# Optimization experiments

Measured on AMD Instinct MI355X. Metric: run time of the kernel, lower is better.

Reference implementation:

```python
import jax, jax.numpy as jnp
import numpy as np

H, W = 3000, 3000

def setup_inputs() -> dict:
    rng = np.random.default_rng(0)
    activities_np = rng.random((H, W)) < 0.9
    nb_active = int(activities_np.sum())
    vertex_weights = jnp.asarray(rng.random((H, W), dtype=np.float32))
    neighbors = jnp.array([(1, 0), (-1, 0), (0, 1), (0, -1)], dtype=jnp.int32)  # rook contiguity
    return {
        "activities": jnp.asarray(activities_np),
        "vertex_weights": vertex_weights,
        "neighbors": neighbors,
        "nb_active": nb_active,
    }


def reference(activities, vertex_weights, neighbors, nb_active):
    nrows, ncols = activities.shape
    num_nodes = nb_active  # static python int
    # active vertex index -> (i, j) coords, row-major order (matches jnp.nonzero)
    rows, cols = jnp.nonzero(activities, size=num_nodes)
    source_xy = jnp.stack([rows, cols], axis=1)  # [N, 2]
    # (i, j) -> active vertex index map, -1 for inactive
    active_map = jnp.full((nrows, ncols), -1, dtype=jnp.int32)
    active_map = active_map.at[rows, cols].set(jnp.arange(num_nodes, dtype=jnp.int32))
    # candidate neighbor coordinates [N, K, 2]
    cand = source_xy[:, None, :] + neighbors[None, :, :].astype(source_xy.dtype)
    ci_raw, cj_raw = cand[..., 0], cand[..., 1]
    in_bounds = (ci_raw >= 0) & (ci_raw < nrows) & (cj_raw >= 0) & (cj_raw < ncols)
    ci = jnp.clip(ci_raw, 0, nrows - 1)
    cj = jnp.clip(cj_raw, 0, ncols - 1)
    target_active = activities[ci, cj]
    valid = in_bounds & target_active  # [N, K]
    # zero out invalid coords before gather (matches original)
    vi = jnp.where(valid, ci_raw, 0)
    vj = jnp.where(valid, cj_raw, 0)
    tgt = jnp.where(valid, active_map[vi, vj], 0)
    src = jnp.where(valid, jnp.arange(num_nodes, dtype=jnp.int32)[:, None], 0)
    vals = jnp.where(valid, vertex_weights[vi, vj], 0.0)
    indices = jnp.stack([src.ravel(), tgt.ravel()], axis=1)  # [N*K, 2]
    return vals.ravel(), indices  # BCOO data and indices, shape (num_nodes, num_nodes)
```

## Files before the change

### kernel.cpp

```cpp
#include <hip/hip_runtime.h>
#include <cstdint>

#define HH 3000
#define WW 3000
#define WPR 48
#define NW (HH * WPR)

typedef unsigned long long u64;
typedef float f4v __attribute__((ext_vector_type(4)));

#define BITS_OFF 0
#define ROWS_OFF 1152000
#define P_OFF    1164032

__device__ __forceinline__ void nt_store4(float a, float b, float c, float d, float4* p) {
    f4v x; x.x = a; x.y = b; x.z = c; x.w = d;
    __builtin_nontemporal_store(x, (f4v*)p);
}

__device__ __forceinline__ int detect_mode(const void* acts, int t, int lane, int wv,
                                           int* s_red, int* s_mode) {
    int v = (int)((const unsigned*)acts)[t];
    #pragma unroll
    for (int off = 32; off > 0; off >>= 1) v = max(v, __shfl_down(v, off));
    if (lane == 0) s_red[wv] = v;
    __syncthreads();
    if (t == 0) {
        int mx = max(max(s_red[0], s_red[1]), max(s_red[2], s_red[3]));
        *s_mode = (mx > 1 && mx <= 0x01010101) ? 1 : 0;
    }
    __syncthreads();
    return *s_mode;
}

__global__ __launch_bounds__(256) void k_build(const void* __restrict__ acts,
                                               u64* __restrict__ bits,
                                               int* __restrict__ rowSums) {
    __shared__ int s_red[4];
    __shared__ int s_mode;
    const int t = threadIdx.x, lane = t & 63, wv = t >> 6;
    const int mode = detect_mode(acts, t, lane, wv, s_red, &s_mode);

    const int r = blockIdx.x;
    const long rowbase = (long)r * WW;
    int mycnt = 0;
    for (int it = 0; it < 12; ++it) {
        int wi = it * 4 + wv;
        int j = wi * 64 + lane;
        bool a = false;
        if (j < WW) {
            if (mode) a = ((const unsigned char*)acts)[rowbase + j] != 0;
            else      a = ((const unsigned*)acts)[rowbase + j] != 0u;
        }
        u64 m = __ballot(a);
        if (lane == 0) {
            bits[r * WPR + wi] = m;
            mycnt += __popcll(m);
        }
    }
    if (lane == 0) s_red[wv] = mycnt;
    __syncthreads();
    if (t == 0) rowSums[r] = s_red[0] + s_red[1] + s_red[2] + s_red[3];
}

__global__ __launch_bounds__(256) void k_prefixP(const u64* __restrict__ bits,
                                                 const int* __restrict__ rowSums,
                                                 int* __restrict__ P) {
    __shared__ int s_red[4];
    const int t = threadIdx.x, lane = t & 63, wv = t >> 6;
    const int r0 = blockIdx.x * 4;
    int s = 0;
    for (int idx = t; idx < r0; idx += 256) s += rowSums[idx];
    #pragma unroll
    for (int off = 32; off > 0; off >>= 1) s += __shfl_down(s, off);
    if (lane == 0) s_red[wv] = s;
    __syncthreads();
    int base = s_red[0] + s_red[1] + s_red[2] + s_red[3];

    const int r = r0 + wv;
    if (r < HH) {
        int rbase = base;
        if (wv >= 1) rbase += rowSums[r0];
        if (wv >= 2) rbase += rowSums[r0 + 1];
        if (wv >= 3) rbase += rowSums[r0 + 2];
        const int w = r * WPR + lane;
        int v = (lane < WPR) ? __popcll(bits[w]) : 0;
        int x = v;
        #pragma unroll
        for (int off = 1; off < 64; off <<= 1) {
            int y = __shfl_up(x, off);
            if (lane >= off) x += y;
        }
        if (lane < WPR) P[w] = rbase + (x - v);
    }
}

__global__ __launch_bounds__(256) void k_emit(const u64* __restrict__ bits,
                                              const int* __restrict__ P,
                                              const float* __restrict__ wts,
                                              float* __restrict__ out, int N) {
    const int t = threadIdx.x;
    const int lane = t & 63;
    const int wv = t >> 6;
    const int i = blockIdx.y;

    float4* valsg = (float4*)out;
    float4* indsg = (float4*)(out + (size_t)N * 4);

    #pragma unroll
    for (int half = 0; half < 2; ++half) {
        const int wi = blockIdx.x * 8 + half * 4 + wv;
        const int j = wi * 64 + lane;
        const int w = i * WPR + wi;
        const u64 mself = bits[w];
        if (!((mself >> lane) & 1ull)) continue;

        const int v = P[w] + __popcll(mself & ((1ull << lane) - 1ull));
        const float nf = (float)v;
        const long c = (long)i * WW + j;

        float val0, val1, val2, val3, sf0, sf1, sf2, sf3, tf0, tf1, tf2, tf3;
        {
            bool ok = (i < HH - 1);
            u64 wd = ok ? bits[w + WPR] : 0ull;
            bool aa = ok && ((wd >> lane) & 1ull);
            val0 = aa ? wts[c + WW] : 0.f; sf0 = aa ? nf : 0.f;
            tf0 = aa ? (float)(P[w + WPR] + __popcll(wd & ((1ull << lane) - 1ull))) : 0.f;
        }
        {
            bool ok = (i > 0);
            u64 wd = ok ? bits[w - WPR] : 0ull;
            bool aa = ok && ((wd >> lane) & 1ull);
            val1 = aa ? wts[c - WW] : 0.f; sf1 = aa ? nf : 0.f;
            tf1 = aa ? (float)(P[w - WPR] + __popcll(wd & ((1ull << lane) - 1ull))) : 0.f;
        }
        {
            bool ok = (j < WW - 1);
            int wn = (lane < 63) ? w : w + 1;
            int b2 = (lane < 63) ? lane + 1 : 0;
            u64 wd = ok ? ((lane < 63) ? mself : bits[wn]) : 0ull;
            bool aa = ok && ((wd >> b2) & 1ull);
            val2 = aa ? wts[c + 1] : 0.f; sf2 = aa ? nf : 0.f;
            tf2 = aa ? (float)(P[wn] + __popcll(wd & ((1ull << b2) - 1ull))) : 0.f;
        }
        {
            bool ok = (j > 0);
            int wn = (lane > 0) ? w : w - 1;
            int b2 = (lane > 0) ? lane - 1 : 63;
            u64 wd = ok ? ((lane > 0) ? mself : bits[wn]) : 0ull;
            bool aa = ok && ((wd >> b2) & 1ull);
            val3 = aa ? wts[c - 1] : 0.f; sf3 = aa ? nf : 0.f;
            tf3 = aa ? (float)(P[wn] + __popcll(wd & ((1ull << b2) - 1ull))) : 0.f;
        }

        nt_store4(val0, val1, val2, val3, &valsg[v]);
        nt_store4(sf0, tf0, sf1, tf1, &indsg[2 * (size_t)v]);
        nt_store4(sf2, tf2, sf3, tf3, &indsg[2 * (size_t)v + 1]);
    }
}

extern "C" void kernel_launch(void* const* d_in, const int* in_sizes, int n_in,
                              void* d_out, int out_size, void* d_ws, size_t ws_size,
                              hipStream_t stream) {
    const void* acts = d_in[0];
    const float* wts = (const float*)d_in[1];
    float* out = (float*)d_out;
    const int N = out_size / 12;

    u64* bits = (u64*)((char*)d_ws + BITS_OFF);
    int* rows = (int*)((char*)d_ws + ROWS_OFF);
    int* P    = (int*)((char*)d_ws + P_OFF);

    k_build<<<HH, 256, 0, stream>>>(acts, bits, rows);
    k_prefixP<<<(HH + 3) / 4, 256, 0, stream>>>(bits, rows, P);
    k_emit<<<dim3(6, HH), 256, 0, stream>>>(bits, P, wts, out, N);
}
```

Baseline: 108.8 us.

## Vectorize bitmask build with 8-byte loads and remap emit blocks per XCD

```diff
diff --git a/kernel.cpp b/kernel.cpp
--- a/kernel.cpp
+++ b/kernel.cpp
@@ -5,6 +5,8 @@
 #define WW 3000
 #define WPR 48
 #define NW (HH * WPR)
+#define NB_EMIT 18000
+#define CHUNK_EMIT (NB_EMIT / 8)
 
 typedef unsigned long long u64;
 typedef float f4v __attribute__((ext_vector_type(4)));
@@ -42,23 +44,38 @@
     const int mode = detect_mode(acts, t, lane, wv, s_red, &s_mode);
 
     const int r = blockIdx.x;
-    const long rowbase = (long)r * WW;
-    int mycnt = 0;
-    for (int it = 0; it < 12; ++it) {
-        int wi = it * 4 + wv;
-        int j = wi * 64 + lane;
-        bool a = false;
-        if (j < WW) {
-            if (mode) a = ((const unsigned char*)acts)[rowbase + j] != 0;
-            else      a = ((const unsigned*)acts)[rowbase + j] != 0u;
+    int rcnt = 0;
+    #pragma unroll
+    for (int it = 0; it < 2; ++it) {
+        const int c0 = it * 2048 + t * 8;
+        u64 m8 = 0;
+        if (c0 < WW) {
+            if (mode) {
+                u64 x = *(const u64*)((const unsigned char*)acts + (long)r * WW + c0);
+                u64 y = x | (x >> 4); y |= y >> 2; y |= y >> 1;
+                y &= 0x0101010101010101ull;
+                m8 = (y * 0x0102040810204080ull) >> 56;
+            } else {
+                const unsigned* p = (const unsigned*)acts + (long)r * WW + c0;
+                uint4 a  = *(const uint4*)p;
+                uint4 b4 = *(const uint4*)(p + 4);
+                m8 = (u64)(a.x  != 0u)        | ((u64)(a.y  != 0u) << 1) |
+                     ((u64)(a.z  != 0u) << 2) | ((u64)(a.w  != 0u) << 3) |
+                     ((u64)(b4.x != 0u) << 4) | ((u64)(b4.y != 0u) << 5) |
+                     ((u64)(b4.z != 0u) << 6) | ((u64)(b4.w != 0u) << 7);
+            }
         }
-        u64 m = __ballot(a);
-        if (lane == 0) {
-            bits[r * WPR + wi] = m;
-            mycnt += __popcll(m);
-        }
+        rcnt += __popcll(m8);
+        u64 word = m8 << (8 * (lane & 7));
+        word |= __shfl_xor(word, 1);
+        word |= __shfl_xor(word, 2);
+        word |= __shfl_xor(word, 4);
+        const int wi = it * 32 + (t >> 3);
+        if ((t & 7) == 0 && wi < WPR) bits[r * WPR + wi] = word;
     }
-    if (lane == 0) s_red[wv] = mycnt;
+    #pragma unroll
+    for (int off = 32; off > 0; off >>= 1) rcnt += __shfl_down(rcnt, off);
+    if (lane == 0) s_red[wv] = rcnt;
     __syncthreads();
     if (t == 0) rowSums[r] = s_red[0] + s_red[1] + s_red[2] + s_red[3];
 }
@@ -102,14 +119,16 @@
     const int t = threadIdx.x;
     const int lane = t & 63;
     const int wv = t >> 6;
-    const int i = blockIdx.y;
+    const int vb = (blockIdx.x & 7) * CHUNK_EMIT + (blockIdx.x >> 3);
+    const int i  = vb / 6;
+    const int bx = vb - i * 6;
 
     float4* valsg = (float4*)out;
     float4* indsg = (float4*)(out + (size_t)N * 4);
 
     #pragma unroll
     for (int half = 0; half < 2; ++half) {
-        const int wi = blockIdx.x * 8 + half * 4 + wv;
+        const int wi = bx * 8 + half * 4 + wv;
         const int j = wi * 64 + lane;
         const int w = i * WPR + wi;
         const u64 mself = bits[w];
@@ -173,5 +192,5 @@
 
     k_build<<<HH, 256, 0, stream>>>(acts, bits, rows);
     k_prefixP<<<(HH + 3) / 4, 256, 0, stream>>>(bits, rows, P);
-    k_emit<<<dim3(6, HH), 256, 0, stream>>>(bits, P, wts, out, N);
+    k_emit<<<NB_EMIT, 256, 0, stream>>>(bits, P, wts, out, N);
 }
```

Result: slower. 126.9 us (+16.6%).
